# Optimization experiments

Hardware: AMD Instinct MI355X
Metric: run time of the kernel (lower is better)

The kernel has to match this reference:

```python
import jax, jax.numpy as jnp
import numpy as np

B, HW, C, H = 4, 2048, 768, 8
HD = C // H  # 96


def _rotate_half_interleaved(t):
    # t: [..., HD]; pairs (t1, t2) at even/odd positions -> (-t2, t1) interleaved
    t1 = t[..., ::2]
    t2 = t[..., 1::2]
    return jnp.stack([-t2, t1], axis=-1).reshape(t.shape)


def setup_inputs() -> dict:
    key = jax.random.key(0)
    kx, kq, kp, kb = jax.random.split(key, 4)
    x = jax.random.normal(kx, (B, HW, C), dtype=jnp.float32)
    # standard interleaved RoPE tables: freq repeated pairwise along head_dim
    inv_freq = 1.0 / (10000.0 ** (np.arange(0, HD, 2, dtype=np.float32) / HD))  # [HD/2]
    angles = np.arange(HW, dtype=np.float32)[:, None] * inv_freq[None, :]        # [HW, HD/2]
    angles = np.repeat(angles, 2, axis=-1)                                        # [HW, HD]
    cos = jnp.asarray(np.cos(angles), dtype=jnp.float32)
    sin = jnp.asarray(np.sin(angles), dtype=jnp.float32)
    Wqkv = jax.random.normal(kq, (3 * C, C), dtype=jnp.float32) * (C ** -0.5)
    Wproj = jax.random.normal(kp, (C, C), dtype=jnp.float32) * (C ** -0.5)
    bproj = jnp.zeros((C,), dtype=jnp.float32)
    return {"x": x, "cos": cos, "sin": sin, "Wqkv": Wqkv, "Wproj": Wproj, "bproj": bproj}


def reference(x, cos, sin, Wqkv, Wproj, bproj):
    Bv, hw, Cv = x.shape
    scale = HD ** -0.5
    qkv = x @ Wqkv.T                                  # [B, hw, 3C]
    qkv = qkv.reshape(Bv, hw, 3, H, HD).transpose(2, 0, 3, 1, 4)  # [3, B, H, hw, HD]
    q, k, v = qkv[0], qkv[1], qkv[2]
    # RoPE: broadcast cos/sin [hw, HD] over [B, H, hw, HD]
    cosb = cos[None, None, :, :]
    sinb = sin[None, None, :, :]
    q = q * cosb + _rotate_half_interleaved(q) * sinb
    k = k * cosb + _rotate_half_interleaved(k) * sinb
    attn = jnp.einsum('bhqd,bhkd->bhqk', q, k) * scale
    attn = jax.nn.softmax(attn, axis=-1)
    out = jnp.einsum('bhqk,bhkd->bhqd', attn, v)      # [B, H, hw, HD]
    out = out.transpose(0, 2, 1, 3).reshape(Bv, hw, Cv)
    return out @ Wproj.T + bproj
```

## Files before the change

### kernel.cpp

```cpp
#include <hip/hip_runtime.h>
#include <hip/hip_bf16.h>
#include <math.h>

#define Bc  4
#define HWc 2048
#define Cc  768
#define Hc  8
#define HDc 96

typedef short bf16x8 __attribute__((ext_vector_type(8)));
typedef float f32x4  __attribute__((ext_vector_type(4)));

static __device__ __forceinline__ unsigned short f2bf(float x) {
    __hip_bfloat16 h = __float2bfloat16(x);
    return *reinterpret_cast<unsigned short*>(&h);
}

#define GLOBAL_AS(p) ((const __attribute__((address_space(1))) void*)(p))
#define LDS_AS(p)    ((__attribute__((address_space(3))) void*)(p))

__global__ __launch_bounds__(256) void cast_all(
    const float* __restrict__ x, const float* __restrict__ Wq,
    const float* __restrict__ Wp, unsigned short* __restrict__ xb,
    unsigned short* __restrict__ Wqb, unsigned short* __restrict__ Wpb,
    int nx4, int nwq4, int nwp4)
{
    int i = blockIdx.x * 256 + threadIdx.x;
    const float* src; unsigned short* dst; int j = i;
    if (i < nx4) { src = x; dst = xb; }
    else if ((j = i - nx4) < nwq4) { src = Wq; dst = Wqb; }
    else if ((j = i - nx4 - nwq4) < nwp4) { src = Wp; dst = Wpb; }
    else return;
    float4 v = ((const float4*)src)[j];
    ushort4 p;
    p.x = f2bf(v.x); p.y = f2bf(v.y); p.z = f2bf(v.z); p.w = f2bf(v.w);
    ((ushort4*)dst)[j] = p;
}

__global__ __launch_bounds__(256) void qkv_mfma_T(
    const unsigned short* __restrict__ Wb, const unsigned short* __restrict__ xb,
    const float* __restrict__ cs, const float* __restrict__ sn,
    unsigned short* __restrict__ qo, unsigned short* __restrict__ ko,
    unsigned short* __restrict__ vt)
{
    __shared__ unsigned short Al[128 * 32];
    __shared__ unsigned short Bl[128 * 32];
    __shared__ unsigned short Tt[64][132];
    const int tid  = threadIdx.x;
    const int lane = tid & 63;
    const int w    = tid >> 6;
    const int c    = lane & 15, qd = lane >> 4;
    const int wm   = w & 1, wn = w >> 1;
    const int m0   = blockIdx.y << 7;
    const int n0   = blockIdx.x << 7;

    const int srow = (w << 5) + (lane >> 2);
    const int sseg = (lane & 3) << 3;
    const unsigned short* Ag = Wb + (size_t)(m0 + srow) * Cc + sseg;
    const unsigned short* Bg = xb + (size_t)(n0 + srow) * Cc + sseg;
    unsigned short* Adst = &Al[(w << 5) * 32];
    unsigned short* Bdst = &Bl[(w << 5) * 32];

    f32x4 acc[4][4];
    #pragma unroll
    for (int i = 0; i < 4; i++)
        #pragma unroll
        for (int j = 0; j < 4; j++) acc[i][j] = (f32x4)0.f;

    for (int k0 = 0; k0 < Cc; k0 += 32) {
        __syncthreads();
        __builtin_amdgcn_global_load_lds(GLOBAL_AS(Ag + k0),            LDS_AS(Adst),            16, 0, 0);
        __builtin_amdgcn_global_load_lds(GLOBAL_AS(Ag + 16 * Cc + k0),  LDS_AS(Adst + 16 * 32),  16, 0, 0);
        __builtin_amdgcn_global_load_lds(GLOBAL_AS(Bg + k0),            LDS_AS(Bdst),            16, 0, 0);
        __builtin_amdgcn_global_load_lds(GLOBAL_AS(Bg + 16 * Cc + k0),  LDS_AS(Bdst + 16 * 32),  16, 0, 0);
        __syncthreads();

        bf16x8 af[4], bfr[4];
        #pragma unroll
        for (int mt = 0; mt < 4; mt++)
            af[mt] = *(const bf16x8*)&Al[((wm << 6) + mt * 16 + c) * 32 + qd * 8];
        #pragma unroll
        for (int nt = 0; nt < 4; nt++)
            bfr[nt] = *(const bf16x8*)&Bl[((wn << 6) + nt * 16 + c) * 32 + qd * 8];
        #pragma unroll
        for (int mt = 0; mt < 4; mt++)
            #pragma unroll
            for (int nt = 0; nt < 4; nt++)
                acc[mt][nt] = __builtin_amdgcn_mfma_f32_16x16x32_bf16(
                    af[mt], bfr[nt], acc[mt][nt], 0, 0, 0);
    }

    const int which = m0 / Cc;
    const int m0l = m0 - which * Cc;
    const float qs = 0.10206207261596577f;

    if (which == 2) {
        #pragma unroll
        for (int mt = 0; mt < 4; mt++) {
            const int c0 = m0l + (wm << 6) + mt * 16 + (qd << 2);
            const int h = c0 / HDc, d = c0 % HDc;
            #pragma unroll
            for (int nt = 0; nt < 4; nt++) {
                const int t = n0 + (wn << 6) + nt * 16 + c;
                const int b = t >> 11, tt = t & (HWc - 1);
                const size_t base = ((size_t)((b * Hc + h) * HDc + d)) * HWc + tt;
                #pragma unroll
                for (int r = 0; r < 4; r++)
                    vt[base + (size_t)r * HWc] = f2bf(acc[mt][nt][r]);
            }
        }
    } else {
        unsigned short* dst = which ? ko : qo;
        const float sc = which ? 1.0f : qs;
        for (int tk = 0; tk < 2; tk++) {
            __syncthreads();
            if (wn == tk) {
                #pragma unroll
                for (int mt = 0; mt < 4; mt++) {
                    const int c0 = m0l + (wm << 6) + mt * 16 + (qd << 2);
                    const int d = c0 % HDc;
                    #pragma unroll
                    for (int nt = 0; nt < 4; nt++) {
                        const int t = n0 + (wn << 6) + nt * 16 + c;
                        const int tt = t & (HWc - 1);
                        const float4 c4 = *(const float4*)&cs[tt * HDc + d];
                        const float4 s4 = *(const float4*)&sn[tt * HDc + d];
                        float o0 = (acc[mt][nt][0] * c4.x - acc[mt][nt][1] * s4.x) * sc;
                        float o1 = (acc[mt][nt][1] * c4.y + acc[mt][nt][0] * s4.y) * sc;
                        float o2 = (acc[mt][nt][2] * c4.z - acc[mt][nt][3] * s4.z) * sc;
                        float o3 = (acc[mt][nt][3] * c4.w + acc[mt][nt][2] * s4.w) * sc;
                        ushort4 pk;
                        pk.x = f2bf(o0); pk.y = f2bf(o1);
                        pk.z = f2bf(o2); pk.w = f2bf(o3);
                        *(ushort4*)&Tt[nt * 16 + c][(wm << 6) + mt * 16 + (qd << 2)] = pk;
                    }
                }
            }
            __syncthreads();
            #pragma unroll
            for (int it = 0; it < 8; it++) {
                int s = tid + (it << 8);
                int row = s >> 5, fseg = (s & 31) << 2;
                int fg = m0l + fseg;
                int h = fg / HDc, d = fg % HDc;
                int token = n0 + tk * 64 + row;
                int b = token >> 11, tt = token & (HWc - 1);
                *(ushort4*)&dst[((size_t)(b * Hc + h) * HWc + tt) * HDc + d] =
                    *(ushort4*)&Tt[row][fseg];
            }
        }
    }
}

__global__ __launch_bounds__(256, 4) void attn_flash(
    const unsigned short* __restrict__ qg, const unsigned short* __restrict__ kg,
    const unsigned short* __restrict__ vtg, unsigned short* __restrict__ ob)
{
    __shared__ unsigned short Ks[64][104];
    __shared__ unsigned short Vt[96][72];
    __shared__ unsigned short Pt[4][16][72];

    const int tid  = threadIdx.x;
    const int lane = tid & 63;
    const int w    = tid >> 6;
    const int c    = lane & 15;
    const int qd   = lane >> 4;
    const int bh   = blockIdx.x;
    const int b    = bh >> 3, h = bh & 7;
    const int q0   = blockIdx.y << 6;

    const unsigned short* kb  = kg  + (size_t)bh * HWc * HDc;
    const unsigned short* vtb = vtg + (size_t)bh * HDc * HWc;

    bf16x8 qt[3];
    {
        const unsigned short* qr = qg + ((size_t)bh * HWc + q0 + w * 16 + c) * HDc + qd * 8;
        #pragma unroll
        for (int ks = 0; ks < 3; ks++)
            qt[ks] = *(const bf16x8*)(qr + ks * 32);
    }

    f32x4 oacc[6];
    #pragma unroll
    for (int mt = 0; mt < 6; mt++) oacc[mt] = (f32x4)0.f;
    float lsum = 0.f;

    for (int ck = 0; ck < 32; ck++) {
        __syncthreads();
        {
            const unsigned short* kc = kb + (size_t)(ck << 6) * HDc;
            #pragma unroll
            for (int it = 0; it < 3; it++) {
                int idx = tid + (it << 8);
                int row = idx / 12, seg = idx - row * 12;
                uint4 val = *(const uint4*)(kc + row * HDc + seg * 8);
                *(uint4*)&Ks[row][seg * 8] = val;
            }
            const unsigned short* vc = vtb + (ck << 6);
            #pragma unroll
            for (int it = 0; it < 3; it++) {
                int idx = tid + (it << 8);
                int row = idx >> 3, seg = idx & 7;
                uint4 val = *(const uint4*)(vc + (size_t)row * HWc + seg * 8);
                *(uint4*)&Vt[row][seg * 8] = val;
            }
        }
        __syncthreads();

        f32x4 sacc[4];
        #pragma unroll
        for (int mt = 0; mt < 4; mt++) sacc[mt] = (f32x4)0.f;
        #pragma unroll
        for (int mt = 0; mt < 4; mt++)
            #pragma unroll
            for (int ks = 0; ks < 3; ks++) {
                bf16x8 af = *(const bf16x8*)&Ks[mt * 16 + c][ks * 32 + qd * 8];
                sacc[mt] = __builtin_amdgcn_mfma_f32_16x16x32_bf16(
                    af, qt[ks], sacc[mt], 0, 0, 0);
            }

        float rs = 0.f;
        #pragma unroll
        for (int mt = 0; mt < 4; mt++)
            #pragma unroll
            for (int r = 0; r < 4; r++) {
                float p = __expf(sacc[mt][r]);
                sacc[mt][r] = p;
                rs += p;
            }
        rs += __shfl_xor(rs, 16);
        rs += __shfl_xor(rs, 32);
        lsum += rs;

        #pragma unroll
        for (int mt = 0; mt < 4; mt++) {
            __hip_bfloat162 p01 = __float22bfloat162_rn(float2{sacc[mt][0], sacc[mt][1]});
            __hip_bfloat162 p23 = __float22bfloat162_rn(float2{sacc[mt][2], sacc[mt][3]});
            uint2 pk;
            pk.x = *reinterpret_cast<unsigned int*>(&p01);
            pk.y = *reinterpret_cast<unsigned int*>(&p23);
            *(uint2*)&Pt[w][c][mt * 16 + qd * 4] = pk;
        }
        bf16x8 pf[2];
        #pragma unroll
        for (int ks = 0; ks < 2; ks++)
            pf[ks] = *(const bf16x8*)&Pt[w][c][ks * 32 + qd * 8];

        #pragma unroll
        for (int mt = 0; mt < 6; mt++)
            #pragma unroll
            for (int ks = 0; ks < 2; ks++) {
                bf16x8 vf = *(const bf16x8*)&Vt[mt * 16 + c][ks * 32 + qd * 8];
                oacc[mt] = __builtin_amdgcn_mfma_f32_16x16x32_bf16(
                    vf, pf[ks], oacc[mt], 0, 0, 0);
            }
    }

    const float linv = 1.0f / lsum;
    unsigned short* orow = ob + ((size_t)(b * HWc + q0 + w * 16 + c)) * Cc + h * HDc;
    #pragma unroll
    for (int mt = 0; mt < 6; mt++) {
        f32x4 val = oacc[mt] * linv;
        ushort4 pk;
        pk.x = f2bf(val[0]); pk.y = f2bf(val[1]);
        pk.z = f2bf(val[2]); pk.w = f2bf(val[3]);
        *(ushort4*)&orow[mt * 16 + qd * 4] = pk;
    }
}

__global__ __launch_bounds__(256) void proj_mfma_T(
    const unsigned short* __restrict__ Wb, const unsigned short* __restrict__ Ab,
    const float* __restrict__ bias, float* __restrict__ out)
{
    __shared__ unsigned short Al[128 * 32];
    __shared__ unsigned short Bl[128 * 32];
    const int tid  = threadIdx.x;
    const int lane = tid & 63;
    const int w    = tid >> 6;
    const int c    = lane & 15, qd = lane >> 4;
    const int wm   = w & 1, wn = w >> 1;
    const int m0   = blockIdx.y << 7;
    const int n0   = blockIdx.x << 7;

    const int srow = (w << 5) + (lane >> 2);
    const int sseg = (lane & 3) << 3;
    const unsigned short* Ag = Wb + (size_t)(m0 + srow) * Cc + sseg;
    const unsigned short* Bg = Ab + (size_t)(n0 + srow) * Cc + sseg;
    unsigned short* Adst = &Al[(w << 5) * 32];
    unsigned short* Bdst = &Bl[(w << 5) * 32];

    f32x4 acc[4][4];
    #pragma unroll
    for (int i = 0; i < 4; i++)
        #pragma unroll
        for (int j = 0; j < 4; j++) acc[i][j] = (f32x4)0.f;

    for (int k0 = 0; k0 < Cc; k0 += 32) {
        __syncthreads();
        __builtin_amdgcn_global_load_lds(GLOBAL_AS(Ag + k0),           LDS_AS(Adst),           16, 0, 0);
        __builtin_amdgcn_global_load_lds(GLOBAL_AS(Ag + 16 * Cc + k0), LDS_AS(Adst + 16 * 32), 16, 0, 0);
        __builtin_amdgcn_global_load_lds(GLOBAL_AS(Bg + k0),           LDS_AS(Bdst),           16, 0, 0);
        __builtin_amdgcn_global_load_lds(GLOBAL_AS(Bg + 16 * Cc + k0), LDS_AS(Bdst + 16 * 32), 16, 0, 0);
        __syncthreads();

        bf16x8 af[4], bfr[4];
        #pragma unroll
        for (int mt = 0; mt < 4; mt++)
            af[mt] = *(const bf16x8*)&Al[((wm << 6) + mt * 16 + c) * 32 + qd * 8];
        #pragma unroll
        for (int nt = 0; nt < 4; nt++)
            bfr[nt] = *(const bf16x8*)&Bl[((wn << 6) + nt * 16 + c) * 32 + qd * 8];
        #pragma unroll
        for (int mt = 0; mt < 4; mt++)
            #pragma unroll
            for (int nt = 0; nt < 4; nt++)
                acc[mt][nt] = __builtin_amdgcn_mfma_f32_16x16x32_bf16(
                    af[mt], bfr[nt], acc[mt][nt], 0, 0, 0);
    }

    #pragma unroll
    for (int mt = 0; mt < 4; mt++) {
        const int f = m0 + (wm << 6) + mt * 16 + (qd << 2);
        const float4 b4 = *(const float4*)&bias[f];
        #pragma unroll
        for (int nt = 0; nt < 4; nt++) {
            const int t = n0 + (wn << 6) + nt * 16 + c;
            float4 val;
            val.x = acc[mt][nt][0] + b4.x;
            val.y = acc[mt][nt][1] + b4.y;
            val.z = acc[mt][nt][2] + b4.z;
            val.w = acc[mt][nt][3] + b4.w;
            *(float4*)&out[(size_t)t * Cc + f] = val;
        }
    }
}

extern "C" void kernel_launch(void* const* d_in, const int* in_sizes, int n_in,
                              void* d_out, int out_size, void* d_ws, size_t ws_size,
                              hipStream_t stream) {
    const float* x     = (const float*)d_in[0];
    const float* cs    = (const float*)d_in[1];
    const float* sn    = (const float*)d_in[2];
    const float* Wqkv  = (const float*)d_in[3];
    const float* Wproj = (const float*)d_in[4];
    const float* bproj = (const float*)d_in[5];
    float* out = (float*)d_out;

    const size_t per = (size_t)Bc * Hc * HWc * HDc;
    const size_t nx  = per;
    const size_t nwq = (size_t)3 * Cc * Cc;
    const size_t nwp = (size_t)Cc * Cc;

    unsigned short* xb  = (unsigned short*)d_ws;
    unsigned short* Wqb = xb + nx;
    unsigned short* Wpb = Wqb + nwq;
    unsigned short* q   = Wpb + nwp;
    unsigned short* k   = q + per;
    unsigned short* vt  = k + per;
    unsigned short* ob  = vt + per;

    const int nx4 = (int)(nx / 4), nwq4 = (int)(nwq / 4), nwp4 = (int)(nwp / 4);
    const int ntot = nx4 + nwq4 + nwp4;
    cast_all<<<dim3((ntot + 255) / 256), 256, 0, stream>>>(
        x, Wqkv, Wproj, xb, Wqb, Wpb, nx4, nwq4, nwp4);

    qkv_mfma_T<<<dim3(64, 18), 256, 0, stream>>>(Wqb, xb, cs, sn, q, k, vt);
    attn_flash<<<dim3(32, 32), 256, 0, stream>>>(q, k, vt, ob);
    proj_mfma_T<<<dim3(64, 6), 256, 0, stream>>>(Wpb, ob, bproj, out);
}
```

Measured before the change: 286.2 us.

## Switch attention to 32x32x16 MFMA with split-KV across warp pairs

Rewrites the attention kernel to use 32x32x16 bf16 MFMA instead of 16x16x32. Each warp now covers 32 queries and half of each 64-key chunk, and the two key halves are summed through LDS at the end. LDS rows are re-padded and read with 8-byte loads to avoid bank conflicts. The aim is fewer MFMA issues and fewer fragment loads from LDS per chunk. The cost is larger accumulator register use and an extra LDS reduction at the end.

```diff
diff --git a/kernel.cpp b/kernel.cpp
--- a/kernel.cpp
+++ b/kernel.cpp
@@ -10,10 +10,19 @@
 
 typedef short bf16x8 __attribute__((ext_vector_type(8)));
 typedef float f32x4  __attribute__((ext_vector_type(4)));
+typedef float f32x16 __attribute__((ext_vector_type(16)));
 
 static __device__ __forceinline__ unsigned short f2bf(float x) {
     __hip_bfloat16 h = __float2bfloat16(x);
     return *reinterpret_cast<unsigned short*>(&h);
+}
+
+static __device__ __forceinline__ bf16x8 ld8(const unsigned short* p) {
+    uint2 lo = *(const uint2*)(p);
+    uint2 hi = *(const uint2*)(p + 4);
+    union { uint4 u; bf16x8 v; } x;
+    x.u.x = lo.x; x.u.y = lo.y; x.u.z = hi.x; x.u.w = hi.y;
+    return x.v;
 }
 
 #define GLOBAL_AS(p) ((const __attribute__((address_space(1))) void*)(p))
@@ -152,19 +161,22 @@
     }
 }
 
-__global__ __launch_bounds__(256, 4) void attn_flash(
+__global__ __launch_bounds__(256, 4) void attn_flash32(
     const unsigned short* __restrict__ qg, const unsigned short* __restrict__ kg,
     const unsigned short* __restrict__ vtg, unsigned short* __restrict__ ob)
 {
-    __shared__ unsigned short Ks[64][104];
-    __shared__ unsigned short Vt[96][72];
-    __shared__ unsigned short Pt[4][16][72];
+    __shared__ __align__(16) unsigned short lds[17536];
+    unsigned short* Ks = lds;
+    unsigned short* Vt = lds + 6400;
+    unsigned short* Pt = lds + 12928;
 
     const int tid  = threadIdx.x;
     const int lane = tid & 63;
     const int w    = tid >> 6;
-    const int c    = lane & 15;
-    const int qd   = lane >> 4;
+    const int qh   = w & 1;
+    const int sh   = w >> 1;
+    const int l31  = lane & 31;
+    const int hk   = lane >> 5;
     const int bh   = blockIdx.x;
     const int b    = bh >> 3, h = bh & 7;
     const int q0   = blockIdx.y << 6;
@@ -172,17 +184,18 @@
     const unsigned short* kb  = kg  + (size_t)bh * HWc * HDc;
     const unsigned short* vtb = vtg + (size_t)bh * HDc * HWc;
 
-    bf16x8 qt[3];
+    bf16x8 qt[6];
     {
-        const unsigned short* qr = qg + ((size_t)bh * HWc + q0 + w * 16 + c) * HDc + qd * 8;
-        #pragma unroll
-        for (int ks = 0; ks < 3; ks++)
-            qt[ks] = *(const bf16x8*)(qr + ks * 32);
-    }
-
-    f32x4 oacc[6];
+        const unsigned short* qr =
+            qg + ((size_t)bh * HWc + q0 + qh * 32 + l31) * HDc + hk * 8;
+        #pragma unroll
+        for (int ks = 0; ks < 6; ks++)
+            qt[ks] = *(const bf16x8*)(qr + ks * 16);
+    }
+
+    f32x16 oacc[3];
     #pragma unroll
-    for (int mt = 0; mt < 6; mt++) oacc[mt] = (f32x4)0.f;
+    for (int mt = 0; mt < 3; mt++) oacc[mt] = (f32x16)0.f;
     float lsum = 0.f;
 
     for (int ck = 0; ck < 32; ck++) {
@@ -193,78 +206,98 @@
             for (int it = 0; it < 3; it++) {
                 int idx = tid + (it << 8);
                 int row = idx / 12, seg = idx - row * 12;
-                uint4 val = *(const uint4*)(kc + row * HDc + seg * 8);
-                *(uint4*)&Ks[row][seg * 8] = val;
+                *(uint4*)&Ks[row * 100 + seg * 8] =
+                    *(const uint4*)(kc + row * HDc + seg * 8);
             }
             const unsigned short* vc = vtb + (ck << 6);
             #pragma unroll
             for (int it = 0; it < 3; it++) {
                 int idx = tid + (it << 8);
                 int row = idx >> 3, seg = idx & 7;
-                uint4 val = *(const uint4*)(vc + (size_t)row * HWc + seg * 8);
-                *(uint4*)&Vt[row][seg * 8] = val;
-            }
-        }
-        __syncthreads();
-
-        f32x4 sacc[4];
-        #pragma unroll
-        for (int mt = 0; mt < 4; mt++) sacc[mt] = (f32x4)0.f;
-        #pragma unroll
-        for (int mt = 0; mt < 4; mt++)
-            #pragma unroll
-            for (int ks = 0; ks < 3; ks++) {
-                bf16x8 af = *(const bf16x8*)&Ks[mt * 16 + c][ks * 32 + qd * 8];
-                sacc[mt] = __builtin_amdgcn_mfma_f32_16x16x32_bf16(
-                    af, qt[ks], sacc[mt], 0, 0, 0);
-            }
+                *(uint4*)&Vt[row * 68 + seg * 8] =
+                    *(const uint4*)(vc + (size_t)row * HWc + seg * 8);
+            }
+        }
+        __syncthreads();
+
+        f32x16 sacc = (f32x16)0.f;
+        #pragma unroll
+        for (int ks = 0; ks < 6; ks++) {
+            bf16x8 af = ld8(&Ks[(sh * 32 + l31) * 100 + ks * 16 + hk * 8]);
+            sacc = __builtin_amdgcn_mfma_f32_32x32x16_bf16(af, qt[ks], sacc, 0, 0, 0);
+        }
 
         float rs = 0.f;
         #pragma unroll
-        for (int mt = 0; mt < 4; mt++)
-            #pragma unroll
-            for (int r = 0; r < 4; r++) {
-                float p = __expf(sacc[mt][r]);
-                sacc[mt][r] = p;
-                rs += p;
-            }
-        rs += __shfl_xor(rs, 16);
+        for (int r = 0; r < 16; r++) {
+            float p = __expf(sacc[r]);
+            sacc[r] = p;
+            rs += p;
+        }
         rs += __shfl_xor(rs, 32);
         lsum += rs;
 
         #pragma unroll
-        for (int mt = 0; mt < 4; mt++) {
-            __hip_bfloat162 p01 = __float22bfloat162_rn(float2{sacc[mt][0], sacc[mt][1]});
-            __hip_bfloat162 p23 = __float22bfloat162_rn(float2{sacc[mt][2], sacc[mt][3]});
+        for (int g = 0; g < 4; g++) {
+            __hip_bfloat162 p01 = __float22bfloat162_rn(
+                float2{sacc[4 * g + 0], sacc[4 * g + 1]});
+            __hip_bfloat162 p23 = __float22bfloat162_rn(
+                float2{sacc[4 * g + 2], sacc[4 * g + 3]});
             uint2 pk;
             pk.x = *reinterpret_cast<unsigned int*>(&p01);
             pk.y = *reinterpret_cast<unsigned int*>(&p23);
-            *(uint2*)&Pt[w][c][mt * 16 + qd * 4] = pk;
+            *(uint2*)&Pt[(w * 32 + l31) * 36 + g * 8 + hk * 4] = pk;
         }
         bf16x8 pf[2];
         #pragma unroll
         for (int ks = 0; ks < 2; ks++)
-            pf[ks] = *(const bf16x8*)&Pt[w][c][ks * 32 + qd * 8];
-
-        #pragma unroll
-        for (int mt = 0; mt < 6; mt++)
+            pf[ks] = ld8(&Pt[(w * 32 + l31) * 36 + ks * 16 + hk * 8]);
+
+        #pragma unroll
+        for (int mt = 0; mt < 3; mt++)
             #pragma unroll
             for (int ks = 0; ks < 2; ks++) {
-                bf16x8 vf = *(const bf16x8*)&Vt[mt * 16 + c][ks * 32 + qd * 8];
-                oacc[mt] = __builtin_amdgcn_mfma_f32_16x16x32_bf16(
+                bf16x8 vf = ld8(&Vt[(mt * 32 + l31) * 68 + sh * 32 + ks * 16 + hk * 8]);
+                oacc[mt] = __builtin_amdgcn_mfma_f32_32x32x16_bf16(
                     vf, pf[ks], oacc[mt], 0, 0, 0);
             }
     }
 
-    const float linv = 1.0f / lsum;
-    unsigned short* orow = ob + ((size_t)(b * HWc + q0 + w * 16 + c)) * Cc + h * HDc;
-    #pragma unroll
-    for (int mt = 0; mt < 6; mt++) {
-        f32x4 val = oacc[mt] * linv;
-        ushort4 pk;
-        pk.x = f2bf(val[0]); pk.y = f2bf(val[1]);
-        pk.z = f2bf(val[2]); pk.w = f2bf(val[3]);
-        *(ushort4*)&orow[mt * 16 + qd * 4] = pk;
+    __syncthreads();
+    float* red = (float*)lds;
+    if (w >= 2) {
+        float* p = red + ((w - 2) * 64 + lane) * 50;
+        #pragma unroll
+        for (int mt = 0; mt < 3; mt++)
+            #pragma unroll
+            for (int r = 0; r < 16; r++)
+                p[mt * 16 + r] = oacc[mt][r];
+        p[48] = lsum;
+    }
+    __syncthreads();
+    if (w < 2) {
+        const float* p = red + (w * 64 + lane) * 50;
+        #pragma unroll
+        for (int mt = 0; mt < 3; mt++)
+            #pragma unroll
+            for (int r = 0; r < 16; r++)
+                oacc[mt][r] += p[mt * 16 + r];
+        lsum += p[48];
+
+        const float linv = 1.0f / lsum;
+        unsigned short* orow =
+            ob + ((size_t)(b * HWc + q0 + qh * 32 + l31)) * Cc + h * HDc;
+        #pragma unroll
+        for (int mt = 0; mt < 3; mt++)
+            #pragma unroll
+            for (int g = 0; g < 4; g++) {
+                ushort4 pk;
+                pk.x = f2bf(oacc[mt][4 * g + 0] * linv);
+                pk.y = f2bf(oacc[mt][4 * g + 1] * linv);
+                pk.z = f2bf(oacc[mt][4 * g + 2] * linv);
+                pk.w = f2bf(oacc[mt][4 * g + 3] * linv);
+                *(ushort4*)&orow[mt * 32 + g * 8 + hk * 4] = pk;
+            }
     }
 }
 
@@ -365,6 +398,6 @@
         x, Wqkv, Wproj, xb, Wqb, Wpb, nx4, nwq4, nwp4);
 
     qkv_mfma_T<<<dim3(64, 18), 256, 0, stream>>>(Wqb, xb, cs, sn, q, k, vt);
-    attn_flash<<<dim3(32, 32), 256, 0, stream>>>(q, k, vt, ob);
+    attn_flash32<<<dim3(32, 32), 256, 0, stream>>>(q, k, vt, ob);
     proj_mfma_T<<<dim3(64, 6), 256, 0, stream>>>(Wpb, ob, bproj, out);
 }
```

New measurement: 300.2 us. +4.9%, slower.
